# Performance work log

Hardware: AMD Instinct MI355X
Metric: run time of the kernel (lower is better)

Reference implementation:

```python
import jax, jax.numpy as jnp
import numpy as np

CHANNELS = 256
C_QK = CHANNELS // 8


def setup_inputs() -> dict:
    key = jax.random.key(0)
    ks = jax.random.split(key, 7)
    b, c, h, w = 8, CHANNELS, 64, 64
    x = jax.random.normal(ks[0], (b, c, h, w), dtype=jnp.float32)
    # 1x1 conv weights stored as [out_ch, in_ch]; biases [out_ch]
    s = 1.0 / np.sqrt(c)
    wq = jax.random.uniform(ks[1], (C_QK, c), jnp.float32, -s, s)
    bq = jax.random.uniform(ks[2], (C_QK,), jnp.float32, -s, s)
    wk = jax.random.uniform(ks[3], (C_QK, c), jnp.float32, -s, s)
    bk = jax.random.uniform(ks[4], (C_QK,), jnp.float32, -s, s)
    wv = jax.random.uniform(ks[5], (c, c), jnp.float32, -s, s)
    bv = jax.random.uniform(ks[6], (c,), jnp.float32, -s, s)
    return {"x": x, "wq": wq, "bq": bq, "wk": wk, "bk": bk, "wv": wv, "bv": bv}


def reference(x, wq, bq, wk, bk, wv, bv):
    b, c, h, w = x.shape
    xf = x.reshape(b, c, h * w)  # [b, c, n]
    # 1x1 convs == per-pixel linear projections
    q = jnp.einsum('oc,bcn->bon', wq, xf) + bq[None, :, None]  # [b, c//8, n]
    k = jnp.einsum('oc,bcn->bon', wk, xf) + bk[None, :, None]  # [b, c//8, n]
    v = jnp.einsum('oc,bcn->bon', wv, xf) + bv[None, :, None]  # [b, c, n]
    # attention[i, j] = q_i . k_j  (no scaling, matching the torch code)
    attn = jnp.einsum('bdi,bdj->bij', q, k)  # [b, n, n]
    attn = jax.nn.softmax(attn, axis=-1)
    # out[:, :, i] = sum_j attn[i, j] * v[:, :, j]
    out = jnp.einsum('bij,bcj->bci', attn, v)  # [b, c, n]
    return out.reshape(b, c, h, w)
```

## Files before the change

### kernel.cpp

```cpp
#include <hip/hip_runtime.h>
#include <stdint.h>

#define NB 8
#define NC 256
#define ND 32
#define NN 4096
#define QT 64
#define KT 32
#define NBUF 3

typedef __attribute__((ext_vector_type(8))) short short8;
typedef __attribute__((ext_vector_type(4))) float float4_;

#define MFMA16(a,b,c) __builtin_amdgcn_mfma_f32_16x16x32_bf16((a),(b),(c),0,0,0)

#if __has_builtin(__builtin_amdgcn_exp2f)
#define EXP2(x) __builtin_amdgcn_exp2f(x)
#else
#define EXP2(x) exp2f(x)
#endif
#define L2E 1.44269504088896f
#define SCB (24.0f * L2E)

__device__ __forceinline__ uint16_t f2bf(float f) {
  uint32_t u = __builtin_bit_cast(uint32_t, f);
  u += 0x7fffu + ((u >> 16) & 1u);
  return (uint16_t)(u >> 16);
}
__device__ __forceinline__ float bf2f(uint16_t h) {
  uint32_t u = (uint32_t)h << 16;
  return __builtin_bit_cast(float, u);
}
__device__ __forceinline__ short8 ld8(const uint16_t* p) {
  return *reinterpret_cast<const short8*>(p);
}
__device__ __forceinline__ void async16(const uint16_t* g, uint16_t* l) {
  __builtin_amdgcn_global_load_lds(
      (const __attribute__((address_space(1))) uint32_t*)g,
      (__attribute__((address_space(3))) uint32_t*)l, 16, 0, 0);
}

__global__ __launch_bounds__(256) void k_prep(
    const float* __restrict__ x, const float* __restrict__ wq,
    const float* __restrict__ wk, const float* __restrict__ wv,
    uint16_t* __restrict__ xTh, uint16_t* __restrict__ xTl,
    uint16_t* __restrict__ Wh, uint16_t* __restrict__ Wl, int use_xl)
{
  int bx = blockIdx.x, tid = threadIdx.x;
  if (bx >= 2048) {
    int e = (bx - 2048) * 256 + tid;
    int r = e >> 8;
    float w = (r < 32) ? wq[e] : (r < 64) ? wk[e - 32 * 256] : wv[e - 64 * 256];
    uint16_t h = f2bf(w);
    Wh[e] = h;
    Wl[e] = f2bf(w - bf2f(h));
    return;
  }
  __shared__ uint32_t tile[64][65];
  int b = bx >> 8, t = bx & 255;
  int c0 = (t >> 6) << 6, n0 = (t & 63) << 6;
  const float* xb = x + ((size_t)b * NC + c0) * NN + n0;
  int cc = tid >> 4, nw = (tid & 15) << 2;
  for (int i = 0; i < 4; i++) {
    int c = cc + 16 * i;
    float4_ v = *reinterpret_cast<const float4_*>(xb + (size_t)c * NN + nw);
    for (int u = 0; u < 4; u++) {
      uint16_t h = f2bf(v[u]);
      uint16_t l = f2bf(v[u] - bf2f(h));
      tile[c][nw + u] = (uint32_t)h | ((uint32_t)l << 16);
    }
  }
  __syncthreads();
  int cw = (tid & 15) << 2, nn = tid >> 4;
  for (int i = 0; i < 4; i++) {
    int n = nn + 16 * i;
    uint32_t p0 = tile[cw + 0][n], p1 = tile[cw + 1][n];
    uint32_t p2 = tile[cw + 2][n], p3 = tile[cw + 3][n];
    size_t o = ((size_t)b * NN + n0 + n) * NC + c0 + cw;
    *(uint32_t*)(xTh + o)     = (p0 & 0xffffu) | (p1 << 16);
    *(uint32_t*)(xTh + o + 2) = (p2 & 0xffffu) | (p3 << 16);
    if (use_xl) {
      *(uint32_t*)(xTl + o)     = (p0 >> 16) | (p1 & 0xffff0000u);
      *(uint32_t*)(xTl + o + 2) = (p2 >> 16) | (p3 & 0xffff0000u);
    }
  }
}

__global__ __launch_bounds__(256) void k_qkv(
    const uint16_t* __restrict__ xTh, const uint16_t* __restrict__ xTl,
    const uint16_t* __restrict__ Wh, const uint16_t* __restrict__ Wl,
    const float* __restrict__ bq, const float* __restrict__ bk,
    const float* __restrict__ bv,
    uint16_t* __restrict__ Qh, uint16_t* __restrict__ Ql,
    uint16_t* __restrict__ Kh, uint16_t* __restrict__ Kl,
    uint16_t* __restrict__ V, int use_xl, int use_lo)
{
  int b = blockIdx.x & 7, n0 = (blockIdx.x >> 3) * 64;
  int tid = threadIdx.x, wid = tid >> 6, lane = tid & 63;
  int l15 = lane & 15, quad = lane >> 4;
  int nb = n0 + wid * 16;
  float4_ acc[20];
  for (int m = 0; m < 20; m++) acc[m] = (float4_){0.f, 0.f, 0.f, 0.f};
  for (int ks = 0; ks < 8; ks++) {
    size_t xa = ((size_t)b * NN + nb + l15) * NC + ks * 32 + quad * 8;
    short8 bh = ld8(xTh + xa);
    short8 blo;
    if (use_xl) blo = ld8(xTl + xa);
    for (int mt = 0; mt < 20; mt++) {
      size_t wa = (size_t)(16 * mt + l15) * NC + ks * 32 + quad * 8;
      short8 ah = ld8(Wh + wa);
      acc[mt] = MFMA16(ah, bh, acc[mt]);
      if (mt < 4) {
        short8 al = ld8(Wl + wa);
        acc[mt] = MFMA16(al, bh, acc[mt]);
      }
      if (use_xl) acc[mt] = MFMA16(ah, blo, acc[mt]);
    }
  }
  int n = nb + l15;
  for (int mt = 0; mt < 20; mt++) {
    for (int r = 0; r < 4; r++) {
      int row = 16 * mt + quad * 4 + r;
      float v = acc[mt][r];
      if (mt < 2) {
        v = (v + bq[row]) * L2E;
        size_t o = ((size_t)b * NN + n) * ND + row;
        uint16_t h = f2bf(v);
        Qh[o] = h;
        if (use_lo) Ql[o] = f2bf(v - bf2f(h));
      } else if (mt < 4) {
        int rk = row - 32;
        v += bk[rk];
        size_t o = ((size_t)b * NN + n) * ND + rk;
        uint16_t h = f2bf(v);
        Kh[o] = h;
        if (use_lo) Kl[o] = f2bf(v - bf2f(h));
      } else {
        int c = row - 64;
        v += bv[c];
        V[((size_t)b * NC + c) * NN + n] = f2bf(v);
      }
    }
  }
}

__global__ __launch_bounds__(512) void k_attn(
    const uint16_t* __restrict__ Qh, const uint16_t* __restrict__ Ql,
    const uint16_t* __restrict__ Kh, const uint16_t* __restrict__ Kl,
    const uint16_t* __restrict__ V, float* __restrict__ out, int use_lo)
{
  __shared__ uint16_t sV[NBUF][256][KT];
  __shared__ uint16_t sP[4][16][40];
  __shared__ float sL[QT];

  int bx = blockIdx.x;
  int b = bx & 7;
  int q0 = (bx >> 3) * QT;
  int tid = threadIdx.x, wid = tid >> 6, lane = tid & 63;
  int l15 = lane & 15, quad = lane >> 4;
  const size_t qkb = (size_t)b * NN * ND;
  const uint16_t* Vb = V + (size_t)b * NC * NN;
  const bool heavy = (wid < 4);

  int sw = (l15 >> 1) & 3;
  auto stageV = [&](int j) {
    int buf = j % NBUF;
    int j0 = j * KT;
    for (int i = 0; i < 4; i++) {
      int sl = (wid - 4) * 256 + 64 * i + lane;
      int c = sl >> 2;
      int q2s = (sl & 3) ^ ((sl >> 3) & 3);
      const uint16_t* g = Vb + (size_t)c * NN + j0 + q2s * 8;
      uint16_t* l = &sV[buf][0][0] + ((wid - 4) * 4 + i) * 512;
      async16(g, l);
    }
  };

  float4_ acc[2][4];
  for (int m = 0; m < 2; m++) for (int n = 0; n < 4; n++)
    acc[m][n] = (float4_){0.f, 0.f, 0.f, 0.f};
  float l_part = 0.f;

  short8 qfh, qfl, kh0, kh1, kl0, kl1;
  if (heavy) {
    size_t a = qkb + (size_t)(q0 + wid * 16 + l15) * ND + quad * 8;
    qfh = ld8(Qh + a);
    if (use_lo) qfl = ld8(Ql + a);
    size_t a0 = qkb + (size_t)l15 * ND + quad * 8;
    size_t a1 = qkb + (size_t)(16 + l15) * ND + quad * 8;
    kh0 = ld8(Kh + a0); kh1 = ld8(Kh + a1);
    if (use_lo) { kl0 = ld8(Kl + a0); kl1 = ld8(Kl + a1); }
  } else {
    stageV(0);
    stageV(1);
  }

  for (int j = 0; j < NN / KT; j++) {
    int buf = j % NBUF;
    if (heavy) {
      short8 nh0, nh1, nl0, nl1;
      if (j < NN / KT - 1) {
        size_t a0 = qkb + (size_t)((j + 1) * KT + l15) * ND + quad * 8;
        size_t a1 = a0 + 16 * ND;
        nh0 = ld8(Kh + a0); nh1 = ld8(Kh + a1);
        if (use_lo) { nl0 = ld8(Kl + a0); nl1 = ld8(Kl + a1); }
      }
      float4_ S0 = (float4_){0.f,0.f,0.f,0.f}, S1 = S0;
      S0 = MFMA16(kh0, qfh, S0);
      S1 = MFMA16(kh1, qfh, S1);
      if (use_lo) {
        S0 = MFMA16(kl0, qfh, S0); S0 = MFMA16(kh0, qfl, S0);
        S1 = MFMA16(kl1, qfh, S1); S1 = MFMA16(kh1, qfl, S1);
      }
      float p0[4], p1[4];
      for (int r = 0; r < 4; r++) {
        p0[r] = EXP2(S0[r] - SCB);
        p1[r] = EXP2(S1[r] - SCB);
      }
      l_part += ((p0[0] + p0[1]) + (p0[2] + p0[3])) +
                ((p1[0] + p1[1]) + (p1[2] + p1[3]));
      uint2 w0, w1;
      w0.x = (uint32_t)f2bf(p0[0]) | ((uint32_t)f2bf(p0[1]) << 16);
      w0.y = (uint32_t)f2bf(p0[2]) | ((uint32_t)f2bf(p0[3]) << 16);
      w1.x = (uint32_t)f2bf(p1[0]) | ((uint32_t)f2bf(p1[1]) << 16);
      w1.y = (uint32_t)f2bf(p1[2]) | ((uint32_t)f2bf(p1[3]) << 16);
      *reinterpret_cast<uint2*>(&sP[wid][l15][4 * quad]) = w0;
      *reinterpret_cast<uint2*>(&sP[wid][l15][16 + 4 * quad]) = w1;
      kh0 = nh0; kh1 = nh1;
      if (use_lo) { kl0 = nl0; kl1 = nl1; }
    } else {
      if (j < NN / KT - 2) stageV(j + 2);
    }
    __syncthreads();
    short8 bfP[4];
    for (int qt = 0; qt < 4; qt++)
      bfP[qt] = ld8(&sP[qt][l15][quad * 8]);
    for (int mt = 0; mt < 2; mt++) {
      short8 af = ld8(&sV[buf][wid * 32 + 16 * mt + l15][(quad ^ sw) * 8]);
      for (int qt = 0; qt < 4; qt++)
        acc[mt][qt] = MFMA16(af, bfP[qt], acc[mt][qt]);
    }
    __syncthreads();
  }

  if (heavy) {
    float l_tot = l_part;
    l_tot += __shfl_xor(l_tot, 16);
    l_tot += __shfl_xor(l_tot, 32);
    if (quad == 0) sL[wid * 16 + l15] = l_tot;
  }
  __syncthreads();
  float linv[4];
  for (int qt = 0; qt < 4; qt++) linv[qt] = 1.0f / sL[qt * 16 + l15];
  for (int mt = 0; mt < 2; mt++)
    for (int qt = 0; qt < 4; qt++)
      for (int r = 0; r < 4; r++) {
        int c = wid * 32 + 16 * mt + quad * 4 + r;
        int q = q0 + qt * 16 + l15;
        out[((size_t)(b * NC + c)) * NN + q] = acc[mt][qt][r] * linv[qt];
      }
}

extern "C" void kernel_launch(void* const* d_in, const int* in_sizes, int n_in,
                              void* d_out, int out_size, void* d_ws, size_t ws_size,
                              hipStream_t stream)
{
  const float* x  = (const float*)d_in[0];
  const float* wq = (const float*)d_in[1];
  const float* bq = (const float*)d_in[2];
  const float* wk = (const float*)d_in[3];
  const float* bk = (const float*)d_in[4];
  const float* wv = (const float*)d_in[5];
  const float* bv = (const float*)d_in[6];
  float* out = (float*)d_out;

  const size_t szXT = (size_t)NB * NN * NC * 2;
  const size_t szW  = (size_t)320 * 256 * 2;
  const size_t szQK = (size_t)NB * NN * ND * 2;
  const size_t szV  = (size_t)NB * NC * NN * 2;
  size_t needA = 2 * szXT + 2 * szW + 4 * szQK + szV;
  size_t needB = szXT + 2 * szW + 4 * szQK + szV;
  int use_xl = ws_size >= needA;
  int use_lo = ws_size >= needB;

  char* p = (char*)d_ws;
  uint16_t* xTh = (uint16_t*)p; p += szXT;
  uint16_t* xTl = use_xl ? (uint16_t*)p : xTh; if (use_xl) p += szXT;
  uint16_t* Wh = (uint16_t*)p; p += szW;
  uint16_t* Wl = (uint16_t*)p; p += szW;
  uint16_t* Qh = (uint16_t*)p; p += szQK;
  uint16_t* Ql = use_lo ? (uint16_t*)p : xTh; if (use_lo) p += szQK;
  uint16_t* Kh = (uint16_t*)p; p += szQK;
  uint16_t* Kl = use_lo ? (uint16_t*)p : xTh; if (use_lo) p += szQK;
  uint16_t* Vw = (uint16_t*)p;

  hipLaunchKernelGGL(k_prep, dim3(2368), dim3(256), 0, stream,
                     x, wq, wk, wv, xTh, xTl, Wh, Wl, use_xl);
  hipLaunchKernelGGL(k_qkv, dim3(512), dim3(256), 0, stream,
                     xTh, xTl, Wh, Wl, bq, bk, bv, Qh, Ql, Kh, Kl, Vw,
                     use_xl, use_lo);
  hipLaunchKernelGGL(k_attn, dim3(512), dim3(512), 0, stream,
                     Qh, Ql, Kh, Kl, Vw, out, use_lo);
}
```

Baseline: 282.9 us.

## Halve attention query tile and split key tile across heavy waves for more blocks

Shrinks the attention query tile from 64 to 32 rows, which doubles the grid to 1024 blocks. The four score-computing waves now split the 32-key tile into two halves per 16-query group, and partial softmax row sums from the two halves are added at the end. V staging drops from triple to double buffering and launch bounds request more resident blocks, aiming at higher occupancy and better spread across CUs. In exchange, every block re-streams all of K and V for half as many queries, which doubles global and LDS traffic per output, and the shallower V pipeline may expose more load latency.

```diff
diff --git a/kernel.cpp b/kernel.cpp
--- a/kernel.cpp
+++ b/kernel.cpp
@@ -5,9 +5,9 @@
 #define NC 256
 #define ND 32
 #define NN 4096
-#define QT 64
+#define QT 32
 #define KT 32
-#define NBUF 3
+#define NBUF 2
 
 typedef __attribute__((ext_vector_type(8))) short short8;
 typedef __attribute__((ext_vector_type(4))) float float4_;
@@ -144,14 +144,14 @@
   }
 }
 
-__global__ __launch_bounds__(512) void k_attn(
+__global__ __launch_bounds__(512, 8) void k_attn(
     const uint16_t* __restrict__ Qh, const uint16_t* __restrict__ Ql,
     const uint16_t* __restrict__ Kh, const uint16_t* __restrict__ Kl,
     const uint16_t* __restrict__ V, float* __restrict__ out, int use_lo)
 {
   __shared__ uint16_t sV[NBUF][256][KT];
-  __shared__ uint16_t sP[4][16][40];
-  __shared__ float sL[QT];
+  __shared__ uint16_t sP[2][16][40];
+  __shared__ float sL[2][2][16];
 
   int bx = blockIdx.x;
   int b = bx & 7;
@@ -161,6 +161,7 @@
   const size_t qkb = (size_t)b * NN * ND;
   const uint16_t* Vb = V + (size_t)b * NC * NN;
   const bool heavy = (wid < 4);
+  const int qg = wid & 1, khalf = wid >> 1;
 
   int sw = (l15 >> 1) & 3;
   auto stageV = [&](int j) {
@@ -176,69 +177,57 @@
     }
   };
 
-  float4_ acc[2][4];
-  for (int m = 0; m < 2; m++) for (int n = 0; n < 4; n++)
+  float4_ acc[2][2];
+  for (int m = 0; m < 2; m++) for (int n = 0; n < 2; n++)
     acc[m][n] = (float4_){0.f, 0.f, 0.f, 0.f};
   float l_part = 0.f;
 
-  short8 qfh, qfl, kh0, kh1, kl0, kl1;
+  short8 qfh, qfl, kh, kl;
   if (heavy) {
-    size_t a = qkb + (size_t)(q0 + wid * 16 + l15) * ND + quad * 8;
+    size_t a = qkb + (size_t)(q0 + qg * 16 + l15) * ND + quad * 8;
     qfh = ld8(Qh + a);
     if (use_lo) qfl = ld8(Ql + a);
-    size_t a0 = qkb + (size_t)l15 * ND + quad * 8;
-    size_t a1 = qkb + (size_t)(16 + l15) * ND + quad * 8;
-    kh0 = ld8(Kh + a0); kh1 = ld8(Kh + a1);
-    if (use_lo) { kl0 = ld8(Kl + a0); kl1 = ld8(Kl + a1); }
+    size_t a0 = qkb + (size_t)(khalf * 16 + l15) * ND + quad * 8;
+    kh = ld8(Kh + a0);
+    if (use_lo) kl = ld8(Kl + a0);
   } else {
     stageV(0);
-    stageV(1);
   }
 
   for (int j = 0; j < NN / KT; j++) {
     int buf = j % NBUF;
     if (heavy) {
-      short8 nh0, nh1, nl0, nl1;
+      short8 nh, nl;
       if (j < NN / KT - 1) {
-        size_t a0 = qkb + (size_t)((j + 1) * KT + l15) * ND + quad * 8;
-        size_t a1 = a0 + 16 * ND;
-        nh0 = ld8(Kh + a0); nh1 = ld8(Kh + a1);
-        if (use_lo) { nl0 = ld8(Kl + a0); nl1 = ld8(Kl + a1); }
-      }
-      float4_ S0 = (float4_){0.f,0.f,0.f,0.f}, S1 = S0;
-      S0 = MFMA16(kh0, qfh, S0);
-      S1 = MFMA16(kh1, qfh, S1);
+        size_t a0 = qkb + (size_t)((j + 1) * KT + khalf * 16 + l15) * ND + quad * 8;
+        nh = ld8(Kh + a0);
+        if (use_lo) nl = ld8(Kl + a0);
+      }
+      float4_ S = (float4_){0.f, 0.f, 0.f, 0.f};
+      S = MFMA16(kh, qfh, S);
       if (use_lo) {
-        S0 = MFMA16(kl0, qfh, S0); S0 = MFMA16(kh0, qfl, S0);
-        S1 = MFMA16(kl1, qfh, S1); S1 = MFMA16(kh1, qfl, S1);
-      }
-      float p0[4], p1[4];
-      for (int r = 0; r < 4; r++) {
-        p0[r] = EXP2(S0[r] - SCB);
-        p1[r] = EXP2(S1[r] - SCB);
-      }
-      l_part += ((p0[0] + p0[1]) + (p0[2] + p0[3])) +
-                ((p1[0] + p1[1]) + (p1[2] + p1[3]));
-      uint2 w0, w1;
-      w0.x = (uint32_t)f2bf(p0[0]) | ((uint32_t)f2bf(p0[1]) << 16);
-      w0.y = (uint32_t)f2bf(p0[2]) | ((uint32_t)f2bf(p0[3]) << 16);
-      w1.x = (uint32_t)f2bf(p1[0]) | ((uint32_t)f2bf(p1[1]) << 16);
-      w1.y = (uint32_t)f2bf(p1[2]) | ((uint32_t)f2bf(p1[3]) << 16);
-      *reinterpret_cast<uint2*>(&sP[wid][l15][4 * quad]) = w0;
-      *reinterpret_cast<uint2*>(&sP[wid][l15][16 + 4 * quad]) = w1;
-      kh0 = nh0; kh1 = nh1;
-      if (use_lo) { kl0 = nl0; kl1 = nl1; }
+        S = MFMA16(kl, qfh, S);
+        S = MFMA16(kh, qfl, S);
+      }
+      float p[4];
+      for (int r = 0; r < 4; r++) p[r] = EXP2(S[r] - SCB);
+      l_part += (p[0] + p[1]) + (p[2] + p[3]);
+      uint2 w0;
+      w0.x = (uint32_t)f2bf(p[0]) | ((uint32_t)f2bf(p[1]) << 16);
+      w0.y = (uint32_t)f2bf(p[2]) | ((uint32_t)f2bf(p[3]) << 16);
+      *reinterpret_cast<uint2*>(&sP[qg][l15][khalf * 16 + 4 * quad]) = w0;
+      kh = nh;
+      if (use_lo) kl = nl;
     } else {
-      if (j < NN / KT - 2) stageV(j + 2);
+      if (j < NN / KT - 1) stageV(j + 1);
     }
     __syncthreads();
-    short8 bfP[4];
-    for (int qt = 0; qt < 4; qt++)
-      bfP[qt] = ld8(&sP[qt][l15][quad * 8]);
+    short8 bfP0 = ld8(&sP[0][l15][quad * 8]);
+    short8 bfP1 = ld8(&sP[1][l15][quad * 8]);
     for (int mt = 0; mt < 2; mt++) {
       short8 af = ld8(&sV[buf][wid * 32 + 16 * mt + l15][(quad ^ sw) * 8]);
-      for (int qt = 0; qt < 4; qt++)
-        acc[mt][qt] = MFMA16(af, bfP[qt], acc[mt][qt]);
+      acc[mt][0] = MFMA16(af, bfP0, acc[mt][0]);
+      acc[mt][1] = MFMA16(af, bfP1, acc[mt][1]);
     }
     __syncthreads();
   }
@@ -247,13 +236,14 @@
     float l_tot = l_part;
     l_tot += __shfl_xor(l_tot, 16);
     l_tot += __shfl_xor(l_tot, 32);
-    if (quad == 0) sL[wid * 16 + l15] = l_tot;
+    if (quad == 0) sL[qg][khalf][l15] = l_tot;
   }
   __syncthreads();
-  float linv[4];
-  for (int qt = 0; qt < 4; qt++) linv[qt] = 1.0f / sL[qt * 16 + l15];
+  float linv[2];
+  for (int qt = 0; qt < 2; qt++)
+    linv[qt] = 1.0f / (sL[qt][0][l15] + sL[qt][1][l15]);
   for (int mt = 0; mt < 2; mt++)
-    for (int qt = 0; qt < 4; qt++)
+    for (int qt = 0; qt < 2; qt++)
       for (int r = 0; r < 4; r++) {
         int c = wid * 32 + 16 * mt + quad * 4 + r;
         int q = q0 + qt * 16 + l15;
@@ -299,6 +289,6 @@
   hipLaunchKernelGGL(k_qkv, dim3(512), dim3(256), 0, stream,
                      xTh, xTl, Wh, Wl, bq, bk, bv, Qh, Ql, Kh, Kl, Vw,
                      use_xl, use_lo);
-  hipLaunchKernelGGL(k_attn, dim3(512), dim3(512), 0, stream,
+  hipLaunchKernelGGL(k_attn, dim3(1024), dim3(512), 0, stream,
                      Qh, Ql, Kh, Kl, Vw, out, use_lo);
 }
```

New measurement: 364.2 us. 28.7% more time.
